# Optimization experiments

Hardware: AMD Instinct MI355X
Metric: run time of the kernel (lower is better)

## Reference

```python
import jax, jax.numpy as jnp
import numpy as np

C = 128
H, W, Z = 128, 128, 16
N_CLASSES = 20


def conv3d(x, w, b, padding='SAME'):
    # x: [B,C,D,H,W], w: [O,I,kd,kh,kw]
    y = jax.lax.conv_general_dilated(x, w, (1, 1, 1), padding,
                                     dimension_numbers=('NCDHW', 'OIDHW', 'NCDHW'))
    return y + b[None, :, None, None, None]


def setup_inputs() -> dict:
    key = jax.random.key(0)
    ks = jax.random.split(key, 16)
    s = lambda fan: 1.0 / np.sqrt(fan)
    inp = {}
    inp['x3d'] = jax.random.normal(ks[0], (1, C, H, W, Z), jnp.float32)
    inp['prob_3d'] = jax.random.uniform(ks[1], (1, 1, H, W, Z), jnp.float32)
    # bottleneck Conv3d(C, C, k=3, pad=1)
    inp['w_bot'] = jax.random.normal(ks[2], (C, C, 3, 3, 3), jnp.float32) * s(C * 27)
    inp['b_bot'] = jnp.zeros((C,), jnp.float32)
    # occ_header: SDB(C -> C//2) approximated as conv3x3 + leaky_relu, then Conv3d(C//2, 2, k=3)
    inp['w_occ1'] = jax.random.normal(ks[3], (C // 2, C, 3, 3, 3), jnp.float32) * s(C * 27)
    inp['b_occ1'] = jnp.zeros((C // 2,), jnp.float32)
    inp['w_occ2'] = jax.random.normal(ks[4], (2, C // 2, 3, 3, 3), jnp.float32) * s(C // 2 * 27)
    inp['b_occ2'] = jnp.zeros((2,), jnp.float32)
    # mlp_prior: Linear(C, C//2) -> LayerNorm -> LeakyReLU -> Linear(C//2, C)
    inp['w_mlp1'] = jax.random.normal(ks[5], (C, C // 2), jnp.float32) * s(C)
    inp['b_mlp1'] = jnp.zeros((C // 2,), jnp.float32)
    inp['ln_g'] = jnp.ones((C // 2,), jnp.float32)
    inp['ln_b'] = jnp.zeros((C // 2,), jnp.float32)
    inp['w_mlp2'] = jax.random.normal(ks[6], (C // 2, C), jnp.float32) * s(C // 2)
    inp['b_mlp2'] = jnp.zeros((C,), jnp.float32)
    # sdb: Conv3d(C, C//2, k=3) + leaky_relu
    inp['w_sdb'] = jax.random.normal(ks[7], (C // 2, C, 3, 3, 3), jnp.float32) * s(C * 27)
    inp['b_sdb'] = jnp.zeros((C // 2,), jnp.float32)
    # ssc_header: Conv3d(C//2, n_classes, k=1)
    inp['w_ssc'] = jax.random.normal(ks[8], (N_CLASSES, C // 2, 1, 1, 1), jnp.float32) * s(C // 2)
    inp['b_ssc'] = jnp.zeros((N_CLASSES,), jnp.float32)
    return inp


def reference(x3d, prob_3d, w_bot, b_bot, w_occ1, b_occ1, w_occ2, b_occ2,
              w_mlp1, b_mlp1, ln_g, ln_b, w_mlp2, b_mlp2, w_sdb, b_sdb,
              w_ssc, b_ssc):
    # dense 3D bottleneck conv
    x = conv3d(x3d, w_bot, b_bot)  # [1,C,H,W,Z]
    # occupancy head on depth-reweighted features
    occ_in = x * prob_3d + x
    occ_h = jax.nn.leaky_relu(conv3d(occ_in, w_occ1, b_occ1))
    occ_logit = conv3d(occ_h, w_occ2, b_occ2)  # [1,2,H,W,Z]
    occ_prob = jax.nn.softmax(occ_logit, axis=1)[:, 1]  # [1,H,W,Z]
    occ_mask = (occ_prob > 0.5).reshape(-1)  # [N]

    # flatten voxel features: [N, C]
    x_flat = x[0].reshape(C, -1).T
    # prior MLP for non-occupied voxels (LayerNorm over feature dim)
    h = x_flat @ w_mlp1 + b_mlp1
    mu = jnp.mean(h, axis=-1, keepdims=True)
    var = jnp.var(h, axis=-1, keepdims=True)
    h = (h - mu) / jnp.sqrt(var + 1e-5) * ln_g + ln_b
    h = jax.nn.leaky_relu(h)
    prior = h @ w_mlp2 + b_mlp2  # [N, C]

    # gather/scatter fused as a masked select:
    # occupied voxels keep seed features, empty voxels take the prior
    vox_flat = jnp.where(occ_mask[:, None], x_flat, prior)  # [N, C]
    vox = vox_flat.T.reshape(1, C, H, W, Z)

    # SDB diffusion conv + SSC head
    d = jax.nn.leaky_relu(conv3d(vox, w_sdb, b_sdb))  # [1,C//2,H,W,Z]
    ssc_logit = conv3d(d, w_ssc, b_ssc)  # [1,20,H,W,Z]
    return ssc_logit
```

## Files before the change

### kernel.cpp

```cpp
#include <hip/hip_runtime.h>

#define AD 128
#define BDW 128
#define ZD 16
#define NVOX (AD*BDW*ZD)
#define SLAB 32768
#define NSLAB 8

typedef __attribute__((ext_vector_type(4))) float f32x4;
typedef __attribute__((ext_vector_type(8))) short bf16x8;
typedef __attribute__((ext_vector_type(4))) short s16x4;

__device__ __forceinline__ float leaky(float v) { return v > 0.f ? v : 0.01f * v; }

__device__ __forceinline__ f32x4 mfma_bf(bf16x8 a, bf16x8 b, f32x4 c) {
    return __builtin_amdgcn_mfma_f32_16x16x32_bf16(a, b, c, 0, 0, 0);
}

__device__ __forceinline__ void split3(float v, unsigned short& s1,
                                       unsigned short& s2, unsigned short& s3) {
    const unsigned u1 = __float_as_uint(v) & 0xFFFF0000u;
    const float r1 = v - __uint_as_float(u1);
    const unsigned u2 = __float_as_uint(r1) & 0xFFFF0000u;
    const float r2 = r1 - __uint_as_float(u2);
    s1 = (unsigned short)(u1 >> 16);
    s2 = (unsigned short)(u2 >> 16);
    s3 = (unsigned short)(__float_as_uint(r2) >> 16);
}

__device__ __forceinline__ int lds_a_off(int v, int chunk) {
    return ((v << 5) + (chunk << 3)) ^ ((v & 7) << 3);
}

__global__ __launch_bounds__(256) void wsplit3(const float* __restrict__ w,
                                               unsigned short* __restrict__ wp, int OC) {
    const int i = blockIdx.x * 256 + threadIdx.x;
    const int PS = OC * 3456;
    if (i >= PS) return;
    const int kp = i & 31;
    const int oc = (i >> 5) % OC;
    const int rest = (i >> 5) / OC;
    const int kb = rest & 3, t = rest >> 2;
    const float v = w[((size_t)oc * 128 + kb * 32 + kp) * 27 + t];
    unsigned short s1, s2, s3;
    split3(v, s1, s2, s3);
    wp[i] = s1; wp[i + PS] = s2; wp[i + 2 * PS] = s3;
}

template<int OC, int PROD, bool PREMUL, bool LEAKY, int RING, bool FUSESSC>
__global__ __launch_bounds__(256, 2) void conv3s(const float* __restrict__ src,
                                              const float* __restrict__ prob,
                                              const unsigned short* __restrict__ W,
                                              const float* __restrict__ bias,
                                              float* __restrict__ out,
                                              const float* __restrict__ wssc,
                                              const float* __restrict__ bssc,
                                              int ablk_base) {
    constexpr int NPL = (PROD == 6) ? 3 : 2;
    constexpr int PLH = 324 * 32;
    __shared__ __align__(16) unsigned short smraw[NPL * PLH];
    unsigned short* sm0 = smraw;
    unsigned short* sm1 = smraw + PLH;
    unsigned short* sm2 = smraw + (NPL - 1) * PLH;

    const int tid = threadIdx.x;
    const int cpx = gridDim.x >> 3;
    const int bx = (blockIdx.x & 7) * cpx + (blockIdx.x >> 3);

    const int ablk = ablk_base + (bx >> 5);
    const int b0   = (bx & 31) * 4;
    const int vblock = ablk * 2048 + b0 * 16;

    const int w = tid >> 6, l = tid & 63;
    const int lo16 = l & 15, hi4 = l >> 4;
    constexpr int NF = (OC == 128) ? 2 : 1;
    constexpr int PS = OC * 3456;
    const int oc_off = w * (16 * NF);

    f32x4 acc0[4][NF], acc1[4][NF];
    const f32x4 z4 = {0.f, 0.f, 0.f, 0.f};
    #pragma unroll
    for (int mf = 0; mf < 4; ++mf)
        #pragma unroll
        for (int nf = 0; nf < NF; ++nf) { acc0[mf][nf] = z4; acc1[mf][nf] = z4; }

    float pf[11][4];
    float pfpm[11];

    #define PREFETCH(KB)                                                          \
        _Pragma("unroll")                                                         \
        for (int it = 0; it < 11; ++it) {                                         \
            const int i = tid + it * 256;                                         \
            float v0 = 0.f, v1 = 0.f, v2 = 0.f, v3 = 0.f, pm = 1.f;               \
            if (i < 2592) {                                                       \
                const int q4 = i / 324;                                           \
                const int v  = i - q4 * 324;                                      \
                const int col = v / 18;                                           \
                const int zz  = v - col * 18;                                     \
                const int ta  = col / 6;                                          \
                const int bi  = col - ta * 6;                                     \
                const int a = ablk + ta - 1;                                      \
                const int b = b0 + bi - 1;                                        \
                const int z = zz - 1;                                             \
                if (((unsigned)a < 128u) && ((unsigned)b < 128u) &&               \
                    ((unsigned)z < 16u)) {                                        \
                    const int q = a * 2048 + b * 16 + z;                          \
                    const float* sp = src + (size_t)((KB) * 32 + q4 * 4) * NVOX + q; \
                    v0 = sp[0]; v1 = sp[(size_t)NVOX];                            \
                    v2 = sp[(size_t)2 * NVOX]; v3 = sp[(size_t)3 * NVOX];         \
                    if (PREMUL) pm = 1.f + prob[q];                               \
                }                                                                 \
            }                                                                     \
            pf[it][0] = v0; pf[it][1] = v1; pf[it][2] = v2; pf[it][3] = v3;       \
            if (PREMUL) pfpm[it] = pm;                                            \
        }

    PREFETCH(0)

    #pragma unroll 1
    for (int kb = 0; kb < 4; ++kb) {
        __syncthreads();
        #pragma unroll
        for (int it = 0; it < 11; ++it) {
            const int i = tid + it * 256;
            if (i < 2592) {
                const int q4 = i / 324;
                const int v  = i - q4 * 324;
                s16x4 t1, t2, t3;
                #pragma unroll
                for (int j = 0; j < 4; ++j) {
                    float f = pf[it][j];
                    if (PREMUL) f *= pfpm[it];
                    unsigned short s1, s2, s3;
                    split3(f, s1, s2, s3);
                    t1[j] = (short)s1; t2[j] = (short)s2; t3[j] = (short)s3;
                }
                const int off = lds_a_off(v, q4 >> 1) + (q4 & 1) * 4;
                *(s16x4*)(sm0 + off) = t1;
                *(s16x4*)(sm1 + off) = t2;
                if (NPL == 3) *(s16x4*)(sm2 + off) = t3;
            }
        }
        if (kb < 3) PREFETCH(kb + 1)
        __syncthreads();

        #pragma unroll 1
        for (int t = 0; t < 27; ++t) {
            const int ta = t / 9, tb = (t / 3) % 3, tz = t % 3;
            const size_t wb = ((size_t)(t * 4 + kb) * OC + oc_off + lo16) * 32 + hi4 * 8;
            bf16x8 b1[NF], b2[NF], b3[NF];
            #pragma unroll
            for (int nf = 0; nf < NF; ++nf) {
                b1[nf] = *(const bf16x8*)(W + wb + nf * 512);
                b2[nf] = *(const bf16x8*)(W + PS + wb + nf * 512);
                if (PROD == 6) b3[nf] = *(const bf16x8*)(W + 2 * PS + wb + nf * 512);
            }
            #pragma unroll
            for (int mf = 0; mf < 4; ++mf) {
                const int v = (ta * 6 + mf + tb) * 18 + lo16 + tz;
                const int ao = lds_a_off(v, hi4);
                const bf16x8 a1 = *(const bf16x8*)(sm0 + ao);
                const bf16x8 a2 = *(const bf16x8*)(sm1 + ao);
                #pragma unroll
                for (int nf = 0; nf < NF; ++nf) {
                    acc0[mf][nf] = mfma_bf(a1, b1[nf], acc0[mf][nf]);
                    acc1[mf][nf] = mfma_bf(a1, b2[nf], acc1[mf][nf]);
                    acc1[mf][nf] = mfma_bf(a2, b1[nf], acc1[mf][nf]);
                }
                if (PROD == 6) {
                    const bf16x8 a3 = *(const bf16x8*)(sm2 + ao);
                    #pragma unroll
                    for (int nf = 0; nf < NF; ++nf) {
                        acc1[mf][nf] = mfma_bf(a2, b2[nf], acc1[mf][nf]);
                        acc1[mf][nf] = mfma_bf(a1, b3[nf], acc1[mf][nf]);
                        acc1[mf][nf] = mfma_bf(a3, b1[nf], acc1[mf][nf]);
                    }
                }
            }
        }
    }
    #undef PREFETCH

    __syncthreads();
    float* ldsT = (float*)smraw;
    #pragma unroll
    for (int mf = 0; mf < 4; ++mf)
        #pragma unroll
        for (int nf = 0; nf < NF; ++nf) {
            const int oc = oc_off + nf * 16 + lo16;
            #pragma unroll
            for (int r = 0; r < 4; ++r) {
                float vv = bias[oc] + acc0[mf][nf][r] + acc1[mf][nf][r];
                if (LEAKY) vv = leaky(vv);
                ldsT[oc * 65 + mf * 16 + hi4 * 4 + r] = vv;
            }
        }
    __syncthreads();
    if (FUSESSC) {
        for (int i = tid; i < 20 * 64; i += 256) {
            const int v = i & 63;
            const int o = i >> 6;
            float acc = bssc[o];
            #pragma unroll
            for (int ic = 0; ic < 64; ++ic)
                acc = fmaf(ldsT[ic * 65 + v], wssc[o * 64 + ic], acc);
            out[(size_t)o * NVOX + vblock + v] = acc;
        }
    } else {
        int ocol;
        if (RING == 0) ocol = vblock;
        else           ocol = ((ablk >> 4) % 3) * SLAB + (vblock & (SLAB - 1));
        const size_t outN = (RING == 0) ? (size_t)NVOX : (size_t)(3 * SLAB);
        for (int i = tid; i < OC * 64; i += 256) {
            const int oc = i >> 6, v = i & 63;
            out[(size_t)oc * outN + ocol + v] = ldsT[oc * 65 + v];
        }
    }
}

__global__ __launch_bounds__(256) void occ2p(const float* __restrict__ HR,
                                             const float* __restrict__ w,
                                             const float* __restrict__ bias,
                                             unsigned char* __restrict__ mask,
                                             int s) {
    __shared__ float wl[3456];
    __shared__ float r0[8][33], r1[8][33];
    const int tid = threadIdx.x;
    for (int i = tid; i < 3456; i += 256) wl[i] = w[i];
    const int v32 = tid & 31, g = tid >> 5;
    const int pl = blockIdx.x * 32 + v32;
    const int p = s * SLAB + pl;
    const int z = p & 15, b = (p >> 4) & 127, a = p >> 11;
    __syncthreads();
    float a0 = 0.f, a1 = 0.f;
    #pragma unroll 1
    for (int t = 0; t < 27; ++t) {
        const int da = t / 9 - 1, db = (t / 3) % 3 - 1, dz = t % 3 - 1;
        if (((unsigned)(a + da) >= 128u) || ((unsigned)(b + db) >= 128u) ||
            ((unsigned)(z + dz) >= 16u)) continue;
        const int q = p + da * 2048 + db * 16 + dz;
        const int col = (((a + da) >> 4) % 3) * SLAB + (q & (SLAB - 1));
        #pragma unroll
        for (int j = 0; j < 8; ++j) {
            const int ic = g * 8 + j;
            const float v = HR[(size_t)ic * (3 * SLAB) + col];
            a0 = fmaf(v, wl[ic * 27 + t], a0);
            a1 = fmaf(v, wl[1728 + ic * 27 + t], a1);
        }
    }
    r0[g][v32] = a0; r1[g][v32] = a1;
    __syncthreads();
    if (g == 0) {
        float t0 = bias[0], t1 = bias[1];
        #pragma unroll
        for (int k = 0; k < 8; ++k) { t0 += r0[k][v32]; t1 += r1[k][v32]; }
        mask[p] = (t1 > t0) ? 1 : 0;
    }
}

__global__ __launch_bounds__(256) void mlp_vox(float* __restrict__ x,
                                               const float* __restrict__ w1,
                                               const float* __restrict__ b1,
                                               const float* __restrict__ g,
                                               const float* __restrict__ beta,
                                               const float* __restrict__ w2,
                                               const float* __restrict__ b2,
                                               const unsigned char* __restrict__ mask) {
    const int p = blockIdx.x * 256 + threadIdx.x;
    float h[64];
    #pragma unroll
    for (int j = 0; j < 64; ++j) h[j] = b1[j];
    #pragma unroll 1
    for (int c = 0; c < 128; ++c) {
        const float xv = x[(size_t)c * NVOX + p];
        #pragma unroll
        for (int j = 0; j < 64; ++j) h[j] = fmaf(xv, w1[c * 64 + j], h[j]);
    }
    float mu = 0.f;
    #pragma unroll
    for (int j = 0; j < 64; ++j) mu += h[j];
    mu *= (1.f / 64.f);
    float var = 0.f;
    #pragma unroll
    for (int j = 0; j < 64; ++j) { const float d = h[j] - mu; var = fmaf(d, d, var); }
    var *= (1.f / 64.f);
    const float rs = rsqrtf(var + 1e-5f);
    #pragma unroll
    for (int j = 0; j < 64; ++j) h[j] = leaky((h[j] - mu) * rs * g[j] + beta[j]);

    const bool m = mask[p] != 0;
    #pragma unroll 1
    for (int c = 0; c < 128; ++c) {
        float pr = b2[c];
        #pragma unroll
        for (int j = 0; j < 64; ++j) pr = fmaf(h[j], w2[j * 128 + c], pr);
        const size_t idx = (size_t)c * NVOX + p;
        x[idx] = m ? x[idx] : pr;
    }
}

extern "C" void kernel_launch(void* const* d_in, const int* in_sizes, int n_in,
                              void* d_out, int out_size, void* d_ws, size_t ws_size,
                              hipStream_t stream) {
    const float* x3d    = (const float*)d_in[0];
    const float* prob   = (const float*)d_in[1];
    const float* w_bot  = (const float*)d_in[2];
    const float* b_bot  = (const float*)d_in[3];
    const float* w_occ1 = (const float*)d_in[4];
    const float* b_occ1 = (const float*)d_in[5];
    const float* w_occ2 = (const float*)d_in[6];
    const float* b_occ2 = (const float*)d_in[7];
    const float* w_mlp1 = (const float*)d_in[8];
    const float* b_mlp1 = (const float*)d_in[9];
    const float* ln_g   = (const float*)d_in[10];
    const float* ln_b   = (const float*)d_in[11];
    const float* w_mlp2 = (const float*)d_in[12];
    const float* b_mlp2 = (const float*)d_in[13];
    const float* w_sdb  = (const float*)d_in[14];
    const float* b_sdb  = (const float*)d_in[15];
    const float* w_ssc  = (const float*)d_in[16];
    const float* b_ssc  = (const float*)d_in[17];

    char* ws = (char*)d_ws;
    float* X32 = (float*)(ws);
    float* HR  = (float*)(ws + 134217728);
    unsigned short* WB3 = (unsigned short*)(ws + 159383552);
    unsigned short* W13 = (unsigned short*)(ws + 162037760);
    unsigned short* WS3 = (unsigned short*)(ws + 163364864);
    unsigned char* mask = (unsigned char*)(ws + 164691968);

    const dim3 blk(256);

    wsplit3<<<1728, blk, 0, stream>>>(w_bot,  WB3, 128);
    wsplit3<<<864,  blk, 0, stream>>>(w_occ1, W13, 64);
    wsplit3<<<864,  blk, 0, stream>>>(w_sdb,  WS3, 64);

    conv3s<128, 6, false, false, 0, false><<<4096, blk, 0, stream>>>(
        x3d, nullptr, WB3, b_bot, X32, nullptr, nullptr, 0);

    for (int s = 0; s < NSLAB; ++s) {
        conv3s<64, 6, true, true, 2, false><<<512, blk, 0, stream>>>(
            X32, prob, W13, b_occ1, HR, nullptr, nullptr, 16 * s);
        if (s >= 1) occ2p<<<1024, blk, 0, stream>>>(HR, w_occ2, b_occ2, mask, s - 1);
    }
    occ2p<<<1024, blk, 0, stream>>>(HR, w_occ2, b_occ2, mask, NSLAB - 1);

    mlp_vox<<<1024, blk, 0, stream>>>(X32, w_mlp1, b_mlp1, ln_g, ln_b, w_mlp2, b_mlp2, mask);

    conv3s<64, 3, false, true, 0, true><<<4096, blk, 0, stream>>>(
        X32, nullptr, WS3, b_sdb, (float*)d_out, w_ssc, b_ssc, 0);
}
```

Measured before the change: 2.554 ms.

## Re-split conv warps over M/N, merge accumulators, stage occ2 halo in LDS

The main conv kernel now splits its four warps 2x2 over voxel fragments and output channels instead of only over channels. Each warp keeps one bias-initialised accumulator set, and the precision-split products all go into that single accumulator. The LDS fill now loads 8 channels per thread and writes 16-byte vectors. The occ2 kernel is rewritten to stage a 64-voxel halo tile of HR in shared memory in two channel halves, cutting redundant global gathers. The cost is a larger shared-memory footprint and fewer blocks in flight. Merging the accumulators serialises more MFMAs on one chain and slightly changes rounding order.

```diff
diff --git a/kernel.cpp b/kernel.cpp
--- a/kernel.cpp
+++ b/kernel.cpp
@@ -9,7 +9,7 @@
 
 typedef __attribute__((ext_vector_type(4))) float f32x4;
 typedef __attribute__((ext_vector_type(8))) short bf16x8;
-typedef __attribute__((ext_vector_type(4))) short s16x4;
+typedef __attribute__((ext_vector_type(8))) short s16x8;
 
 __device__ __forceinline__ float leaky(float v) { return v > 0.f ? v : 0.01f * v; }
 
@@ -73,28 +73,32 @@
 
     const int w = tid >> 6, l = tid & 63;
     const int lo16 = l & 15, hi4 = l >> 4;
-    constexpr int NF = (OC == 128) ? 2 : 1;
+    const int wm = w >> 1, wo = w & 1;
+    constexpr int NF = OC / 32;
     constexpr int PS = OC * 3456;
-    const int oc_off = w * (16 * NF);
-
-    f32x4 acc0[4][NF], acc1[4][NF];
-    const f32x4 z4 = {0.f, 0.f, 0.f, 0.f};
-    #pragma unroll
-    for (int mf = 0; mf < 4; ++mf)
-        #pragma unroll
-        for (int nf = 0; nf < NF; ++nf) { acc0[mf][nf] = z4; acc1[mf][nf] = z4; }
-
-    float pf[11][4];
-    float pfpm[11];
+    const int oc_off = wo * (OC / 2);
+
+    f32x4 acc[2][NF];
+    #pragma unroll
+    for (int nf = 0; nf < NF; ++nf) {
+        const float bv = bias[oc_off + nf * 16 + lo16];
+        acc[0][nf] = f32x4{bv, bv, bv, bv};
+        acc[1][nf] = f32x4{bv, bv, bv, bv};
+    }
+
+    float pf[6][8];
+    float pfpm[6];
 
     #define PREFETCH(KB)                                                          \
         _Pragma("unroll")                                                         \
-        for (int it = 0; it < 11; ++it) {                                         \
+        for (int it = 0; it < 6; ++it) {                                          \
             const int i = tid + it * 256;                                         \
-            float v0 = 0.f, v1 = 0.f, v2 = 0.f, v3 = 0.f, pm = 1.f;               \
-            if (i < 2592) {                                                       \
-                const int q4 = i / 324;                                           \
-                const int v  = i - q4 * 324;                                      \
+            _Pragma("unroll")                                                     \
+            for (int j = 0; j < 8; ++j) pf[it][j] = 0.f;                          \
+            pfpm[it] = 1.f;                                                       \
+            if (i < 1296) {                                                       \
+                const int q8 = i / 324;                                           \
+                const int v  = i - q8 * 324;                                      \
                 const int col = v / 18;                                           \
                 const int zz  = v - col * 18;                                     \
                 const int ta  = col / 6;                                          \
@@ -105,14 +109,12 @@
                 if (((unsigned)a < 128u) && ((unsigned)b < 128u) &&               \
                     ((unsigned)z < 16u)) {                                        \
                     const int q = a * 2048 + b * 16 + z;                          \
-                    const float* sp = src + (size_t)((KB) * 32 + q4 * 4) * NVOX + q; \
-                    v0 = sp[0]; v1 = sp[(size_t)NVOX];                            \
-                    v2 = sp[(size_t)2 * NVOX]; v3 = sp[(size_t)3 * NVOX];         \
-                    if (PREMUL) pm = 1.f + prob[q];                               \
+                    const float* sp = src + (size_t)((KB) * 32 + q8 * 8) * NVOX + q; \
+                    _Pragma("unroll")                                             \
+                    for (int j = 0; j < 8; ++j) pf[it][j] = sp[(size_t)j * NVOX]; \
+                    if (PREMUL) pfpm[it] = 1.f + prob[q];                         \
                 }                                                                 \
             }                                                                     \
-            pf[it][0] = v0; pf[it][1] = v1; pf[it][2] = v2; pf[it][3] = v3;       \
-            if (PREMUL) pfpm[it] = pm;                                            \
         }
 
     PREFETCH(0)
@@ -121,24 +123,24 @@
     for (int kb = 0; kb < 4; ++kb) {
         __syncthreads();
         #pragma unroll
-        for (int it = 0; it < 11; ++it) {
+        for (int it = 0; it < 6; ++it) {
             const int i = tid + it * 256;
-            if (i < 2592) {
-                const int q4 = i / 324;
-                const int v  = i - q4 * 324;
-                s16x4 t1, t2, t3;
+            if (i < 1296) {
+                const int q8 = i / 324;
+                const int v  = i - q8 * 324;
+                s16x8 t1, t2, t3;
                 #pragma unroll
-                for (int j = 0; j < 4; ++j) {
+                for (int j = 0; j < 8; ++j) {
                     float f = pf[it][j];
                     if (PREMUL) f *= pfpm[it];
                     unsigned short s1, s2, s3;
                     split3(f, s1, s2, s3);
                     t1[j] = (short)s1; t2[j] = (short)s2; t3[j] = (short)s3;
                 }
-                const int off = lds_a_off(v, q4 >> 1) + (q4 & 1) * 4;
-                *(s16x4*)(sm0 + off) = t1;
-                *(s16x4*)(sm1 + off) = t2;
-                if (NPL == 3) *(s16x4*)(sm2 + off) = t3;
+                const int off = lds_a_off(v, q8);
+                *(s16x8*)(sm0 + off) = t1;
+                *(s16x8*)(sm1 + off) = t2;
+                if (NPL == 3) *(s16x8*)(sm2 + off) = t3;
             }
         }
         if (kb < 3) PREFETCH(kb + 1)
@@ -147,33 +149,34 @@
         #pragma unroll 1
         for (int t = 0; t < 27; ++t) {
             const int ta = t / 9, tb = (t / 3) % 3, tz = t % 3;
-            const size_t wb = ((size_t)(t * 4 + kb) * OC + oc_off + lo16) * 32 + hi4 * 8;
             bf16x8 b1[NF], b2[NF], b3[NF];
             #pragma unroll
             for (int nf = 0; nf < NF; ++nf) {
-                b1[nf] = *(const bf16x8*)(W + wb + nf * 512);
-                b2[nf] = *(const bf16x8*)(W + PS + wb + nf * 512);
-                if (PROD == 6) b3[nf] = *(const bf16x8*)(W + 2 * PS + wb + nf * 512);
-            }
-            #pragma unroll
-            for (int mf = 0; mf < 4; ++mf) {
-                const int v = (ta * 6 + mf + tb) * 18 + lo16 + tz;
+                const size_t wb = ((size_t)(t * 4 + kb) * OC + oc_off + nf * 16 + lo16) * 32 + hi4 * 8;
+                b1[nf] = *(const bf16x8*)(W + wb);
+                b2[nf] = *(const bf16x8*)(W + PS + wb);
+                if (PROD == 6) b3[nf] = *(const bf16x8*)(W + 2 * PS + wb);
+            }
+            #pragma unroll
+            for (int mf = 0; mf < 2; ++mf) {
+                const int f = wm * 2 + mf;
+                const int v = (ta * 6 + f + tb) * 18 + lo16 + tz;
                 const int ao = lds_a_off(v, hi4);
                 const bf16x8 a1 = *(const bf16x8*)(sm0 + ao);
                 const bf16x8 a2 = *(const bf16x8*)(sm1 + ao);
                 #pragma unroll
                 for (int nf = 0; nf < NF; ++nf) {
-                    acc0[mf][nf] = mfma_bf(a1, b1[nf], acc0[mf][nf]);
-                    acc1[mf][nf] = mfma_bf(a1, b2[nf], acc1[mf][nf]);
-                    acc1[mf][nf] = mfma_bf(a2, b1[nf], acc1[mf][nf]);
+                    acc[mf][nf] = mfma_bf(a1, b1[nf], acc[mf][nf]);
+                    acc[mf][nf] = mfma_bf(a1, b2[nf], acc[mf][nf]);
+                    acc[mf][nf] = mfma_bf(a2, b1[nf], acc[mf][nf]);
                 }
                 if (PROD == 6) {
                     const bf16x8 a3 = *(const bf16x8*)(sm2 + ao);
                     #pragma unroll
                     for (int nf = 0; nf < NF; ++nf) {
-                        acc1[mf][nf] = mfma_bf(a2, b2[nf], acc1[mf][nf]);
-                        acc1[mf][nf] = mfma_bf(a1, b3[nf], acc1[mf][nf]);
-                        acc1[mf][nf] = mfma_bf(a3, b1[nf], acc1[mf][nf]);
+                        acc[mf][nf] = mfma_bf(a2, b2[nf], acc[mf][nf]);
+                        acc[mf][nf] = mfma_bf(a1, b3[nf], acc[mf][nf]);
+                        acc[mf][nf] = mfma_bf(a3, b1[nf], acc[mf][nf]);
                     }
                 }
             }
@@ -184,15 +187,15 @@
     __syncthreads();
     float* ldsT = (float*)smraw;
     #pragma unroll
-    for (int mf = 0; mf < 4; ++mf)
+    for (int mf = 0; mf < 2; ++mf)
         #pragma unroll
         for (int nf = 0; nf < NF; ++nf) {
             const int oc = oc_off + nf * 16 + lo16;
             #pragma unroll
             for (int r = 0; r < 4; ++r) {
-                float vv = bias[oc] + acc0[mf][nf][r] + acc1[mf][nf][r];
+                float vv = acc[mf][nf][r];
                 if (LEAKY) vv = leaky(vv);
-                ldsT[oc * 65 + mf * 16 + hi4 * 4 + r] = vv;
+                ldsT[oc * 65 + (wm * 2 + mf) * 16 + hi4 * 4 + r] = vv;
             }
         }
     __syncthreads();
@@ -200,11 +203,11 @@
         for (int i = tid; i < 20 * 64; i += 256) {
             const int v = i & 63;
             const int o = i >> 6;
-            float acc = bssc[o];
+            float acc2 = bssc[o];
             #pragma unroll
             for (int ic = 0; ic < 64; ++ic)
-                acc = fmaf(ldsT[ic * 65 + v], wssc[o * 64 + ic], acc);
-            out[(size_t)o * NVOX + vblock + v] = acc;
+                acc2 = fmaf(ldsT[ic * 65 + v], wssc[o * 64 + ic], acc2);
+            out[(size_t)o * NVOX + vblock + v] = acc2;
         }
     } else {
         int ocol;
@@ -218,43 +221,70 @@
     }
 }
 
-__global__ __launch_bounds__(256) void occ2p(const float* __restrict__ HR,
-                                             const float* __restrict__ w,
-                                             const float* __restrict__ bias,
-                                             unsigned char* __restrict__ mask,
-                                             int s) {
+__global__ __launch_bounds__(256, 2) void occ2s(const float* __restrict__ HR,
+                                                const float* __restrict__ w,
+                                                const float* __restrict__ bias,
+                                                unsigned char* __restrict__ mask,
+                                                int s) {
+    __shared__ float hl[324 * 36];
     __shared__ float wl[3456];
-    __shared__ float r0[8][33], r1[8][33];
+    __shared__ float red0[4][66], red1[4][66];
+
     const int tid = threadIdx.x;
     for (int i = tid; i < 3456; i += 256) wl[i] = w[i];
-    const int v32 = tid & 31, g = tid >> 5;
-    const int pl = blockIdx.x * 32 + v32;
-    const int p = s * SLAB + pl;
-    const int z = p & 15, b = (p >> 4) & 127, a = p >> 11;
-    __syncthreads();
+
+    const int p0 = s * SLAB + blockIdx.x * 64;
+    const int a0r = p0 >> 11;
+    const int bb0 = (p0 >> 4) & 127;
+    const int g = tid >> 6, v64 = tid & 63;
+
     float a0 = 0.f, a1 = 0.f;
     #pragma unroll 1
-    for (int t = 0; t < 27; ++t) {
-        const int da = t / 9 - 1, db = (t / 3) % 3 - 1, dz = t % 3 - 1;
-        if (((unsigned)(a + da) >= 128u) || ((unsigned)(b + db) >= 128u) ||
-            ((unsigned)(z + dz) >= 16u)) continue;
-        const int q = p + da * 2048 + db * 16 + dz;
-        const int col = (((a + da) >> 4) % 3) * SLAB + (q & (SLAB - 1));
-        #pragma unroll
-        for (int j = 0; j < 8; ++j) {
-            const int ic = g * 8 + j;
-            const float v = HR[(size_t)ic * (3 * SLAB) + col];
-            a0 = fmaf(v, wl[ic * 27 + t], a0);
-            a1 = fmaf(v, wl[1728 + ic * 27 + t], a1);
-        }
-    }
-    r0[g][v32] = a0; r1[g][v32] = a1;
+    for (int half = 0; half < 2; ++half) {
+        __syncthreads();
+        for (int i = tid; i < 2592; i += 256) {
+            const int q4 = i / 324;
+            const int v  = i - q4 * 324;
+            const int col = v / 18;
+            const int zz  = v - col * 18;
+            const int ta  = col / 6;
+            const int bi  = col - ta * 6;
+            const int a = a0r + ta - 1;
+            const int b = bb0 + bi - 1;
+            const int z = zz - 1;
+            f32x4 val = {0.f, 0.f, 0.f, 0.f};
+            if (((unsigned)a < 128u) && ((unsigned)b < 128u) && ((unsigned)z < 16u)) {
+                const int q = a * 2048 + b * 16 + z;
+                const int rc = ((a >> 4) % 3) * SLAB + (q & (SLAB - 1));
+                const int ic0 = half * 32 + q4 * 4;
+                #pragma unroll
+                for (int j = 0; j < 4; ++j)
+                    val[j] = HR[(size_t)(ic0 + j) * (3 * SLAB) + rc];
+            }
+            *(f32x4*)(hl + v * 36 + q4 * 4) = val;
+        }
+        __syncthreads();
+        #pragma unroll 1
+        for (int t = 0; t < 27; ++t) {
+            const int ta = t / 9, tb = (t / 3) % 3, tz = t % 3;
+            const int vt = (ta * 6 + (v64 >> 4) + tb) * 18 + (v64 & 15) + tz;
+            #pragma unroll
+            for (int j = 0; j < 8; ++j) {
+                const int icl = g * 8 + j;
+                const int ic = half * 32 + icl;
+                const float hh = hl[vt * 36 + icl];
+                a0 = fmaf(hh, wl[ic * 27 + t], a0);
+                a1 = fmaf(hh, wl[1728 + ic * 27 + t], a1);
+            }
+        }
+    }
+    red0[g][v64] = a0; red1[g][v64] = a1;
     __syncthreads();
     if (g == 0) {
         float t0 = bias[0], t1 = bias[1];
         #pragma unroll
-        for (int k = 0; k < 8; ++k) { t0 += r0[k][v32]; t1 += r1[k][v32]; }
-        mask[p] = (t1 > t0) ? 1 : 0;
+        for (int k = 0; k < 4; ++k) { t0 += red0[k][v64]; t1 += red1[k][v64]; }
+        mask[p0 + v64] = (t1 > t0) ? 1 : 0;
     }
 }
 
@@ -341,9 +371,9 @@
     for (int s = 0; s < NSLAB; ++s) {
         conv3s<64, 6, true, true, 2, false><<<512, blk, 0, stream>>>(
             X32, prob, W13, b_occ1, HR, nullptr, nullptr, 16 * s);
-        if (s >= 1) occ2p<<<1024, blk, 0, stream>>>(HR, w_occ2, b_occ2, mask, s - 1);
-    }
-    occ2p<<<1024, blk, 0, stream>>>(HR, w_occ2, b_occ2, mask, NSLAB - 1);
+        if (s >= 1) occ2s<<<512, blk, 0, stream>>>(HR, w_occ2, b_occ2, mask, s - 1);
+    }
+    occ2s<<<512, blk, 0, stream>>>(HR, w_occ2, b_occ2, mask, NSLAB - 1);
 
     mlp_vox<<<1024, blk, 0, stream>>>(X32, w_mlp1, b_mlp1, ln_g, ln_b, w_mlp2, b_mlp2, mask);
 
```

Measured after the change: 2.919 ms. +14.3%, slower.
